# Kernel tuning notes

Hardware: AMD Instinct MI355X
Metric: run time of the kernel (lower is better)

The kernel has to match this reference:

```python
import jax, jax.numpy as jnp
import numpy as np

NUM_NODES = 50000
NUM_EDGES = 800000
IN_DIM = 64
HIDDEN = 64
NUM_EDGE_TYPES = 6


def leaky_relu(x, alpha=0.2):
    return jnp.maximum(alpha * x, x)


def setup_inputs() -> dict:
    key = jax.random.key(0)
    ks = jax.random.split(key, 8)
    inputs = jax.random.normal(ks[0], (NUM_NODES, IN_DIM), dtype=jnp.float32)
    source_indices = jax.random.randint(ks[1], (NUM_EDGES,), 0, NUM_NODES)
    dest_indices = jax.random.randint(ks[2], (NUM_EDGES,), 0, NUM_NODES)
    edge_types = jax.random.randint(ks[3], (NUM_EDGES,), 0, NUM_EDGE_TYPES)
    # params: xavier-ish dense kernels, tiny biases, uniform edge-type embedding
    W1 = jax.random.normal(ks[4], (IN_DIM, HIDDEN), dtype=jnp.float32) * (1.0 / np.sqrt(IN_DIM))
    b1 = jnp.zeros((HIDDEN,), dtype=jnp.float32)
    W2 = jax.random.normal(ks[5], (2 * HIDDEN, 1), dtype=jnp.float32) * (1.0 / np.sqrt(2 * HIDDEN))
    b2 = jnp.zeros((1,), dtype=jnp.float32)
    edge_emb = jax.random.uniform(ks[6], (NUM_EDGE_TYPES, HIDDEN), dtype=jnp.float32, minval=-0.1, maxval=0.1)
    return {
        "inputs": inputs,
        "source_indices": source_indices,
        "dest_indices": dest_indices,
        "edge_types": edge_types,
        "num_nodes": NUM_NODES,
        "W1": W1,
        "b1": b1,
        "W2": W2,
        "b2": b2,
        "edge_emb": edge_emb,
    }


def reference(inputs, source_indices, dest_indices, edge_types, num_nodes, W1, b1, W2, b2, edge_emb):
    # keys == queries == values in this layer
    keys = inputs @ W1 + b1                      # [N, H]
    ee = edge_emb[edge_types]                    # [E, H]
    keys_source = keys[source_indices]           # [E, H]
    queries_dest = keys[dest_indices]            # [E, H]
    wh = jnp.concatenate([keys_source + ee, queries_dest], axis=-1)  # [E, 2H]
    logits = leaky_relu(wh @ W2 + b2)            # [E, 1]
    # segment softmax over destination nodes (empty segments never gathered)
    seg_max = jax.ops.segment_max(logits, dest_indices, num_segments=num_nodes)  # [N, 1]
    exp_logits = jnp.exp(logits - seg_max[dest_indices])
    exp_sum = jax.ops.segment_sum(exp_logits, dest_indices, num_segments=num_nodes)
    attn = exp_logits / exp_sum[dest_indices]    # [E, 1]
    weighted = (keys_source + ee) * attn         # [E, H]  (values_source == keys_source)
    outputs = jax.ops.segment_sum(weighted, dest_indices, num_segments=num_nodes)  # [N, H]
    return outputs
```

## Files before the change

kernel.cpp:

```cpp
#include <hip/hip_runtime.h>
#include <hip/hip_bf16.h>
#include <hip/hip_fp16.h>


__device__ __forceinline__ unsigned short f2bf(float f) {
    unsigned u = __float_as_uint(f);
    u += 0x7FFFu + ((u >> 16) & 1u);
    return (unsigned short)(u >> 16);
}
__device__ __forceinline__ float bf2f(unsigned short h) {
    return __uint_as_float(((unsigned)h) << 16);
}

#define NBLK_H 256
#define CAPB   16384

__global__ __launch_bounds__(256) void k_nodes(
    const float* __restrict__ inputs, const float* __restrict__ W1,
    const float* __restrict__ b1, const float* __restrict__ W2,
    const float* __restrict__ edge_emb, const int* __restrict__ dst,
    unsigned short* __restrict__ keys, float* __restrict__ alpha_src,
    float* __restrict__ alpha_dst, float* __restrict__ alpha_ee,
    int* __restrict__ histG, int N, int E, int NB, int chunk)
{
    __shared__ float W1s[64 * 64];
    __shared__ float W2s[128];
    __shared__ float xs[16 * 65];
    __shared__ int histL[256];

    const int t = threadIdx.x;
    const int row0 = blockIdx.x * 16;

    const float4* W1g = reinterpret_cast<const float4*>(W1);
    float4* W1sv = reinterpret_cast<float4*>(W1s);
#pragma unroll
    for (int i = 0; i < 4; i++) W1sv[t + 256 * i] = W1g[t + 256 * i];
    if (t < 128) W2s[t] = W2[t];

#pragma unroll
    for (int i = 0; i < 4; i++) {
        int idx = t + 256 * i;
        int r = idx >> 6, c = idx & 63;
        if (row0 + r < N)
            xs[r * 65 + c] = inputs[(size_t)(row0 + r) * 64 + c];
    }
    __syncthreads();

    const int lane = t & 63;
    const int wave = t >> 6;
    const int rl = wave * 4 + (lane >> 4);
    const int j4 = lane & 15;
    const int row = row0 + rl;

    const float4* W1v = reinterpret_cast<const float4*>(W1s);
    float4 acc = {0.f, 0.f, 0.f, 0.f};
#pragma unroll
    for (int k = 0; k < 64; k++) {
        float a = xs[rl * 65 + k];
        float4 w = W1v[k * 16 + j4];
        acc.x += a * w.x; acc.y += a * w.y; acc.z += a * w.z; acc.w += a * w.w;
    }

    if (row < N) {
        float4 bv = reinterpret_cast<const float4*>(b1)[j4];
        acc.x += bv.x; acc.y += bv.y; acc.z += bv.z; acc.w += bv.w;
        ushort4 kv;
        kv.x = f2bf(acc.x); kv.y = f2bf(acc.y);
        kv.z = f2bf(acc.z); kv.w = f2bf(acc.w);
        reinterpret_cast<ushort4*>(keys)[(size_t)row * 16 + j4] = kv;

        float p1 = acc.x * W2s[4 * j4]      + acc.y * W2s[4 * j4 + 1]
                 + acc.z * W2s[4 * j4 + 2]  + acc.w * W2s[4 * j4 + 3];
        float p2 = acc.x * W2s[64 + 4 * j4]     + acc.y * W2s[64 + 4 * j4 + 1]
                 + acc.z * W2s[64 + 4 * j4 + 2] + acc.w * W2s[64 + 4 * j4 + 3];
#pragma unroll
        for (int m = 8; m >= 1; m >>= 1) {
            p1 += __shfl_xor(p1, m);
            p2 += __shfl_xor(p2, m);
        }
        if (j4 == 0) { alpha_src[row] = p1; alpha_dst[row] = p2; }
    }

    if (blockIdx.x == 0 && t < 6) {
        float s = 0.f;
        for (int c = 0; c < 64; c++) s += edge_emb[t * 64 + c] * W2s[c];
        alpha_ee[t] = s;
    }

    if (blockIdx.x < NBLK_H) {
        const int blk = blockIdx.x;
        for (int b = t; b < NB; b += 256) histL[b] = 0;
        __syncthreads();
        const int lim = min(E, (blk + 1) * chunk);
        for (int e = blk * chunk + t; e < lim; e += 256)
            atomicAdd(&histL[dst[e] >> 8], 1);
        __syncthreads();
        for (int b = t; b < NB; b += 256)
            histG[b * NBLK_H + blk] = histL[b];
    }
}

__global__ __launch_bounds__(256) void k_scanA(
    int* __restrict__ histG, int* __restrict__ bsum)
{
    __shared__ int sm[256];
    const int t = threadIdx.x;
    const int b = blockIdx.x;
    int v = histG[b * NBLK_H + t];
    sm[t] = v;
    __syncthreads();
    for (int off = 1; off < 256; off <<= 1) {
        int x = 0;
        if (t >= off) x = sm[t - off];
        __syncthreads();
        if (t >= off) sm[t] += x;
        __syncthreads();
    }
    histG[b * NBLK_H + t] = sm[t] - v;
    if (t == 255) bsum[b] = sm[255];
}

__global__ __launch_bounds__(256) void k_scanB(
    const int* __restrict__ bsum, int* __restrict__ boff, int NB)
{
    __shared__ int sm[256];
    const int t = threadIdx.x;
    sm[t] = (t < NB) ? bsum[t] : 0;
    __syncthreads();
    for (int off = 1; off < 256; off <<= 1) {
        int x = 0;
        if (t >= off) x = sm[t - off];
        __syncthreads();
        if (t >= off) sm[t] += x;
        __syncthreads();
    }
    if (t < NB) boff[t] = (t == 0) ? 0 : sm[t - 1];
    if (t == 255) boff[NB] = sm[255];
}

__global__ __launch_bounds__(256) void k_bucket_scatter(
    const int* __restrict__ src, const int* __restrict__ dst,
    const int* __restrict__ ety, const int* __restrict__ histG,
    const int* __restrict__ boff, int* __restrict__ ebuf,
    int E, int NB, int chunk)
{
    extern __shared__ int cur[];
    const int t = threadIdx.x;
    const int blk = blockIdx.x;
    for (int b = t; b < NB; b += 256) cur[b] = boff[b] + histG[b * NBLK_H + blk];
    __syncthreads();
    const int lim = min(E, (blk + 1) * chunk);
    for (int e = blk * chunk + t; e < lim; e += 256) {
        int d = dst[e];
        int pos = atomicAdd(&cur[d >> 8], 1);
        ebuf[pos] = src[e] | (ety[e] << 16) | ((d & 255) << 19);
    }
}

__global__ __launch_bounds__(256) void k_localcsr(
    int* __restrict__ ebuf, const int* __restrict__ boff,
    const float* __restrict__ a_src, const float* __restrict__ a_dst,
    const float* __restrict__ a_ee, const float* __restrict__ b2,
    int* __restrict__ rp, __half* __restrict__ wexp,
    float* __restrict__ dsum, int N, int NB, int E)
{
    __shared__ int   estage[CAPB];
    __shared__ int   h[256];
    __shared__ int   sm[256];
    __shared__ int   cur2[256];
    __shared__ float fsum[256];
    __shared__ float baseL[256];
    __shared__ float aeeL[8];

    const int t = threadIdx.x;
    const int b = blockIdx.x;
    const int begB = boff[b];
    const int endB = boff[b + 1];
    const int cnt = endB - begB;
    const int idx = (b << 8) + t;

    h[t] = 0;
    fsum[t] = 0.f;
    baseL[t] = (idx < N) ? (a_dst[idx] + b2[0]) : 0.f;
    if (t < 6) aeeL[t] = a_ee[t];
    __syncthreads();

    for (int i = t; i < cnt; i += 256) {
        int r = ebuf[begB + i];
        if (i < CAPB) estage[i] = r;
        atomicAdd(&h[(r >> 19) & 255], 1);
    }
    __syncthreads();

    sm[t] = h[t];
    __syncthreads();
    for (int off = 1; off < 256; off <<= 1) {
        int x = 0;
        if (t >= off) x = sm[t - off];
        __syncthreads();
        if (t >= off) sm[t] += x;
        __syncthreads();
    }
    int lstart = (t == 0) ? 0 : sm[t - 1];

    if (idx < N) rp[idx] = begB + lstart;
    if (b == NB - 1 && t == 0) rp[N] = E;
    cur2[t] = begB + lstart;
    __syncthreads();

    for (int i = t; i < cnt; i += 256) {
        int r = (i < CAPB) ? estage[i] : ebuf[begB + i];
        int s  = r & 0xFFFF;
        int ty = (r >> 16) & 7;
        int dl = (r >> 19) & 255;
        float l = a_src[s] + aeeL[ty] + baseL[dl];
        l = fmaxf(0.2f * l, l);
        float w = expf(l);
        int pos = atomicAdd(&cur2[dl], 1);
        ebuf[pos] = r & 0x7FFFF;
        wexp[pos] = __float2half_rn(w);
        atomicAdd(&fsum[dl], w);
    }
    __syncthreads();
    if (idx < N) dsum[idx] = fsum[t];
}

__global__ __launch_bounds__(256) void k_out(
    const int* __restrict__ rp, const int* __restrict__ erec,
    const __half* __restrict__ wexp, const float* __restrict__ dsum,
    const unsigned short* __restrict__ keys, const float* __restrict__ edge_emb,
    float* __restrict__ out, int N)
{
    __shared__ float ee4[384];
    __shared__ int   srec[4][64];
    __shared__ float sw[4][64];

    const int t = threadIdx.x;
    for (int i = t; i < 384; i += 256) ee4[i] = edge_emb[i];
    __syncthreads();

    const int lane = t & 63;
    const int wid  = t >> 6;
    const int d = blockIdx.x * 4 + wid;
    if (d >= N) return;

    const int beg = rp[d], end = rp[d + 1];
    const float inv = (end > beg) ? 1.f / dsum[d] : 0.f;

    const int g  = lane >> 4;
    const int j4 = lane & 15;
    const float4* ee4v = reinterpret_cast<const float4*>(ee4);
    float4 acc = {0.f, 0.f, 0.f, 0.f};

    for (int cbase = beg; cbase < end; cbase += 64) {
        const int n = min(64, end - cbase);
        if (lane < n) {
            srec[wid][lane] = erec[cbase + lane];
            sw[wid][lane]   = __half2float(wexp[cbase + lane]);
        }
        __builtin_amdgcn_wave_barrier();
        for (int j = g; j < n; j += 4) {
            int   r = srec[wid][j];
            float w = sw[wid][j];
            int s0 = r & 0xFFFF, ty = r >> 16;
            ushort4 kv = reinterpret_cast<const ushort4*>(keys)[(size_t)s0 * 16 + j4];
            float4  ev = ee4v[ty * 16 + j4];
            acc.x += (bf2f(kv.x) + ev.x) * w;
            acc.y += (bf2f(kv.y) + ev.y) * w;
            acc.z += (bf2f(kv.z) + ev.z) * w;
            acc.w += (bf2f(kv.w) + ev.w) * w;
        }
        __builtin_amdgcn_wave_barrier();
    }

#pragma unroll
    for (int m = 16; m <= 32; m <<= 1) {
        acc.x += __shfl_xor(acc.x, m);
        acc.y += __shfl_xor(acc.y, m);
        acc.z += __shfl_xor(acc.z, m);
        acc.w += __shfl_xor(acc.w, m);
    }
    if (g == 0) {
        acc.x *= inv; acc.y *= inv; acc.z *= inv; acc.w *= inv;
        reinterpret_cast<float4*>(out)[(size_t)d * 16 + j4] = acc;
    }
}

extern "C" void kernel_launch(void* const* d_in, const int* in_sizes, int n_in,
                              void* d_out, int out_size, void* d_ws, size_t ws_size,
                              hipStream_t stream) {
    const float* inputs   = (const float*)d_in[0];
    const int*   src      = (const int*)d_in[1];
    const int*   dst      = (const int*)d_in[2];
    const int*   ety      = (const int*)d_in[3];
    const float* W1       = (const float*)d_in[5];
    const float* b1       = (const float*)d_in[6];
    const float* W2       = (const float*)d_in[7];
    const float* b2       = (const float*)d_in[8];
    const float* edge_emb = (const float*)d_in[9];
    float* out = (float*)d_out;

    const int N  = in_sizes[0] / 64;
    const int E  = in_sizes[1];
    const int NB = (N + 255) >> 8;
    const int M  = NB * NBLK_H;
    const int chunk = (E + NBLK_H - 1) / NBLK_H;

    float*          ws      = (float*)d_ws;
    unsigned short* keys    = (unsigned short*)ws;
    float*          a_src   = ws + (size_t)N * 32;
    float*          a_dst   = a_src + N;
    float*          a_ee    = a_dst + N;
    int*            rp      = (int*)(a_ee + 8);
    int*            histG   = rp + (N + 2);
    int*            bsum    = histG + M;
    int*            boff    = bsum + 256;
    int*            ebuf    = boff + 256;
    __half*         wexp    = (__half*)(ebuf + E);
    float*          dsum    = (float*)(wexp + ((E + 1) & ~1));

    int nblk = (N + 15) / 16;
    k_nodes<<<nblk, 256, 0, stream>>>(inputs, W1, b1, W2, edge_emb, dst,
                                      keys, a_src, a_dst, a_ee, histG, N, E, NB, chunk);
    k_scanA<<<NB, 256, 0, stream>>>(histG, bsum);
    k_scanB<<<1, 256, 0, stream>>>(bsum, boff, NB);
    k_bucket_scatter<<<NBLK_H, 256, NB * sizeof(int), stream>>>(src, dst, ety, histG,
                                                                boff, ebuf, E, NB, chunk);
    k_localcsr<<<NB, 256, 0, stream>>>(ebuf, boff, a_src, a_dst, a_ee, b2,
                                       rp, wexp, dsum, N, NB, E);
    k_out<<<(N + 3) / 4, 256, 0, stream>>>(rp, ebuf, wexp, dsum, keys, edge_emb, out, N);
}
```

Before: 85.32 us.

## Fold block-offset scan into scatter and CSR kernels, unroll output gather

Removes the single-block k_scanB launch. The scatter and local-CSR kernels now each redo the 256-entry prefix scan over bucket sums in shared memory, which saves one kernel launch and one global round trip. The output aggregation loop is unrolled by two with two independent accumulators, so two key gathers can be in flight at once. In exchange, every block repeats a small scan, and the aggregation uses more registers.

After: 83.14 us. -2.6%, faster.

```diff
diff --git a/kernel.cpp b/kernel.cpp
--- a/kernel.cpp
+++ b/kernel.cpp
@@ -120,12 +120,19 @@
     if (t == 255) bsum[b] = sm[255];
 }
 
-__global__ __launch_bounds__(256) void k_scanB(
-    const int* __restrict__ bsum, int* __restrict__ boff, int NB)
+__global__ __launch_bounds__(256) void k_bucket_scatter(
+    const int* __restrict__ src, const int* __restrict__ dst,
+    const int* __restrict__ ety, const int* __restrict__ histG,
+    const int* __restrict__ bsum, int* __restrict__ ebuf,
+    int E, int NB, int chunk)
 {
     __shared__ int sm[256];
-    const int t = threadIdx.x;
-    sm[t] = (t < NB) ? bsum[t] : 0;
+    __shared__ int cur[256];
+    const int t = threadIdx.x;
+    const int blk = blockIdx.x;
+
+    int bs = (t < NB) ? bsum[t] : 0;
+    sm[t] = bs;
     __syncthreads();
     for (int off = 1; off < 256; off <<= 1) {
         int x = 0;
@@ -134,21 +141,9 @@
         if (t >= off) sm[t] += x;
         __syncthreads();
     }
-    if (t < NB) boff[t] = (t == 0) ? 0 : sm[t - 1];
-    if (t == 255) boff[NB] = sm[255];
-}
-
-__global__ __launch_bounds__(256) void k_bucket_scatter(
-    const int* __restrict__ src, const int* __restrict__ dst,
-    const int* __restrict__ ety, const int* __restrict__ histG,
-    const int* __restrict__ boff, int* __restrict__ ebuf,
-    int E, int NB, int chunk)
-{
-    extern __shared__ int cur[];
-    const int t = threadIdx.x;
-    const int blk = blockIdx.x;
-    for (int b = t; b < NB; b += 256) cur[b] = boff[b] + histG[b * NBLK_H + blk];
-    __syncthreads();
+    if (t < NB) cur[t] = (sm[t] - bs) + histG[t * NBLK_H + blk];
+    __syncthreads();
+
     const int lim = min(E, (blk + 1) * chunk);
     for (int e = blk * chunk + t; e < lim; e += 256) {
         int d = dst[e];
@@ -158,7 +153,7 @@
 }
 
 __global__ __launch_bounds__(256) void k_localcsr(
-    int* __restrict__ ebuf, const int* __restrict__ boff,
+    int* __restrict__ ebuf, const int* __restrict__ bsum,
     const float* __restrict__ a_src, const float* __restrict__ a_dst,
     const float* __restrict__ a_ee, const float* __restrict__ b2,
     int* __restrict__ rp, __half* __restrict__ wexp,
@@ -174,10 +169,22 @@
 
     const int t = threadIdx.x;
     const int b = blockIdx.x;
-    const int begB = boff[b];
-    const int endB = boff[b + 1];
-    const int cnt = endB - begB;
     const int idx = (b << 8) + t;
+
+    int bs = (t < NB) ? bsum[t] : 0;
+    sm[t] = bs;
+    __syncthreads();
+    for (int off = 1; off < 256; off <<= 1) {
+        int x = 0;
+        if (t >= off) x = sm[t - off];
+        __syncthreads();
+        if (t >= off) sm[t] += x;
+        __syncthreads();
+    }
+    const int begB = (b == 0) ? 0 : sm[b - 1];
+    const int endB = sm[b];
+    const int cnt  = endB - begB;
+    __syncthreads();
 
     h[t] = 0;
     fsum[t] = 0.f;
@@ -250,7 +257,8 @@
     const int g  = lane >> 4;
     const int j4 = lane & 15;
     const float4* ee4v = reinterpret_cast<const float4*>(ee4);
-    float4 acc = {0.f, 0.f, 0.f, 0.f};
+    float4 acc0 = {0.f, 0.f, 0.f, 0.f};
+    float4 acc1 = {0.f, 0.f, 0.f, 0.f};
 
     for (int cbase = beg; cbase < end; cbase += 64) {
         const int n = min(64, end - cbase);
@@ -259,20 +267,43 @@
             sw[wid][lane]   = __half2float(wexp[cbase + lane]);
         }
         __builtin_amdgcn_wave_barrier();
-        for (int j = g; j < n; j += 4) {
-            int   r = srec[wid][j];
-            float w = sw[wid][j];
-            int s0 = r & 0xFFFF, ty = r >> 16;
-            ushort4 kv = reinterpret_cast<const ushort4*>(keys)[(size_t)s0 * 16 + j4];
-            float4  ev = ee4v[ty * 16 + j4];
-            acc.x += (bf2f(kv.x) + ev.x) * w;
-            acc.y += (bf2f(kv.y) + ev.y) * w;
-            acc.z += (bf2f(kv.z) + ev.z) * w;
-            acc.w += (bf2f(kv.w) + ev.w) * w;
+        int j = g;
+        for (; j + 4 < n; j += 8) {
+            int   r0 = srec[wid][j];
+            int   r1 = srec[wid][j + 4];
+            float w0 = sw[wid][j];
+            float w1 = sw[wid][j + 4];
+            int sA = r0 & 0xFFFF, tyA = r0 >> 16;
+            int sB = r1 & 0xFFFF, tyB = r1 >> 16;
+            ushort4 kv0 = reinterpret_cast<const ushort4*>(keys)[(size_t)sA * 16 + j4];
+            ushort4 kv1 = reinterpret_cast<const ushort4*>(keys)[(size_t)sB * 16 + j4];
+            float4  ev0 = ee4v[tyA * 16 + j4];
+            float4  ev1 = ee4v[tyB * 16 + j4];
+            acc0.x += (bf2f(kv0.x) + ev0.x) * w0;
+            acc0.y += (bf2f(kv0.y) + ev0.y) * w0;
+            acc0.z += (bf2f(kv0.z) + ev0.z) * w0;
+            acc0.w += (bf2f(kv0.w) + ev0.w) * w0;
+            acc1.x += (bf2f(kv1.x) + ev1.x) * w1;
+            acc1.y += (bf2f(kv1.y) + ev1.y) * w1;
+            acc1.z += (bf2f(kv1.z) + ev1.z) * w1;
+            acc1.w += (bf2f(kv1.w) + ev1.w) * w1;
+        }
+        if (j < n) {
+            int   r0 = srec[wid][j];
+            float w0 = sw[wid][j];
+            int sA = r0 & 0xFFFF, tyA = r0 >> 16;
+            ushort4 kv0 = reinterpret_cast<const ushort4*>(keys)[(size_t)sA * 16 + j4];
+            float4  ev0 = ee4v[tyA * 16 + j4];
+            acc0.x += (bf2f(kv0.x) + ev0.x) * w0;
+            acc0.y += (bf2f(kv0.y) + ev0.y) * w0;
+            acc0.z += (bf2f(kv0.z) + ev0.z) * w0;
+            acc0.w += (bf2f(kv0.w) + ev0.w) * w0;
         }
         __builtin_amdgcn_wave_barrier();
     }
 
+    float4 acc = { acc0.x + acc1.x, acc0.y + acc1.y,
+                   acc0.z + acc1.z, acc0.w + acc1.w };
 #pragma unroll
     for (int m = 16; m <= 32; m <<= 1) {
         acc.x += __shfl_xor(acc.x, m);
@@ -314,8 +345,7 @@
     int*            rp      = (int*)(a_ee + 8);
     int*            histG   = rp + (N + 2);
     int*            bsum    = histG + M;
-    int*            boff    = bsum + 256;
-    int*            ebuf    = boff + 256;
+    int*            ebuf    = bsum + 256;
     __half*         wexp    = (__half*)(ebuf + E);
     float*          dsum    = (float*)(wexp + ((E + 1) & ~1));
 
@@ -323,10 +353,9 @@
     k_nodes<<<nblk, 256, 0, stream>>>(inputs, W1, b1, W2, edge_emb, dst,
                                       keys, a_src, a_dst, a_ee, histG, N, E, NB, chunk);
     k_scanA<<<NB, 256, 0, stream>>>(histG, bsum);
-    k_scanB<<<1, 256, 0, stream>>>(bsum, boff, NB);
-    k_bucket_scatter<<<NBLK_H, 256, NB * sizeof(int), stream>>>(src, dst, ety, histG,
-                                                                boff, ebuf, E, NB, chunk);
-    k_localcsr<<<NB, 256, 0, stream>>>(ebuf, boff, a_src, a_dst, a_ee, b2,
+    k_bucket_scatter<<<NBLK_H, 256, 0, stream>>>(src, dst, ety, histG,
+                                                 bsum, ebuf, E, NB, chunk);
+    k_localcsr<<<NB, 256, 0, stream>>>(ebuf, bsum, a_src, a_dst, a_ee, b2,
                                        rp, wexp, dsum, N, NB, E);
     k_out<<<(N + 3) / 4, 256, 0, stream>>>(rp, ebuf, wexp, dsum, keys, edge_emb, out, N);
 }
```
